# Performance work log

Measured on AMD Instinct MI355X. Metric: run time of the kernel, lower is better.

## Reference

```python
import jax, jax.numpy as jnp
import numpy as np

B, T, E, H, V, C, L = 32, 512, 512, 512, 50000, 32, 2


def _lstm_dir(x, Wih, Whh, bih, bhh, reverse):
    # x: (B,T,in). Precompute the big input GEMM once; scan only does h @ Whh^T.
    xw = jnp.einsum('bti,gi->btg', x, Wih) + bih + bhh  # (B,T,4H)
    Hd = Whh.shape[1]
    Bd = x.shape[0]

    def step(carry, xt):
        h, c = carry
        g = xt + h @ Whh.T
        i, f, gg, o = jnp.split(g, 4, axis=-1)  # torch gate order i,f,g,o
        c = jax.nn.sigmoid(f) * c + jax.nn.sigmoid(i) * jnp.tanh(gg)
        h = jax.nn.sigmoid(o) * jnp.tanh(c)
        return (h, c), h

    init = (jnp.zeros((Bd, Hd), x.dtype), jnp.zeros((Bd, Hd), x.dtype))
    _, hs = jax.lax.scan(step, init, jnp.swapaxes(xw, 0, 1), reverse=reverse)
    return jnp.swapaxes(hs, 0, 1)  # (B,T,H), time-aligned for both directions


def setup_inputs() -> dict:
    key = jax.random.key(0)
    keys = jax.random.split(key, 40)

    def u(k, shape, scale):
        return jax.random.uniform(k, shape, jnp.float32, -scale, scale)

    s = 1.0 / np.sqrt(H)
    inp = {
        'x': jax.random.randint(keys[0], (B, T), 0, V),
        'truth': jax.random.uniform(keys[1], (B, T, 1), jnp.float32),
        'teacher_forcing': 1,
        'emb': jax.random.normal(keys[2], (V, E), jnp.float32),
    }
    ki = 3
    for l in range(L):
        insz = E if l == 0 else 2 * H
        for d in ('f', 'b'):
            inp[f'Wih{l}{d}'] = u(keys[ki], (4 * H, insz), s); ki += 1
            inp[f'Whh{l}{d}'] = u(keys[ki], (4 * H, H), s); ki += 1
            inp[f'bih{l}{d}'] = u(keys[ki], (4 * H,), s); ki += 1
            inp[f'bhh{l}{d}'] = u(keys[ki], (4 * H,), s); ki += 1
    sc = 1.0 / np.sqrt(2 * H + 1)
    inp['Wc'] = u(keys[ki], (C, 2 * H + 1), sc); ki += 1
    inp['bc'] = u(keys[ki], (C,), sc)
    return inp


def reference(x, truth, teacher_forcing, emb,
              Wih0f, Whh0f, bih0f, bhh0f, Wih0b, Whh0b, bih0b, bhh0b,
              Wih1f, Whh1f, bih1f, bhh1f, Wih1b, Whh1b, bih1b, bhh1b,
              Wc, bc):
    h = emb[x]  # (B,T,E)
    layer_params = [
        ((Wih0f, Whh0f, bih0f, bhh0f), (Wih0b, Whh0b, bih0b, bhh0b)),
        ((Wih1f, Whh1f, bih1f, bhh1f), (Wih1b, Whh1b, bih1b, bhh1b)),
    ]
    for pf, pb in layer_params:
        out_f = _lstm_dir(h, *pf, reverse=False)
        out_b = _lstm_dir(h, *pb, reverse=True)
        h = jnp.concatenate([out_f, out_b], axis=-1)  # (B,T,2H)
    # past feature: zeros at t=0; truth[:, t-1] when teacher forcing, else zeros
    zero0 = jnp.zeros((h.shape[0], 1, 1), h.dtype)
    if teacher_forcing:
        past = jnp.concatenate([zero0, truth[:, :-1, :]], axis=1)  # (B,T,1)
    else:
        past = jnp.zeros((h.shape[0], h.shape[1], 1), h.dtype)
    feat = jnp.concatenate([past, h], axis=-1)  # (B,T,2H+1)
    logits = jnp.einsum('btf,cf->btc', feat, Wc) + bc
    y = jax.nn.log_softmax(logits, axis=-1)  # softmax over classes (intended math)
    return jnp.swapaxes(y, 1, 2)  # (B, classes, T)
```

## Files before the change

### kernel.cpp

```cpp
#include <hip/hip_runtime.h>


#define BB 32
#define TT 512
#define EE 512
#define HH 512
#define NG 2048
#define CC 32

typedef __attribute__((ext_vector_type(8))) short short8v;
typedef __attribute__((ext_vector_type(4))) float float4v;
typedef unsigned long long u64;

__device__ __forceinline__ float bf2f(unsigned short u) {
    return __uint_as_float(((unsigned)u) << 16);
}
__device__ __forceinline__ float bf_lo(unsigned u) { return __uint_as_float(u << 16); }
__device__ __forceinline__ float bf_hi(unsigned u) { return __uint_as_float(u & 0xffff0000u); }
__device__ __forceinline__ unsigned short f2bf(float f) {
    unsigned u = __float_as_uint(f);
    u += 0x7fffu + ((u >> 16) & 1u);
    return (unsigned short)(u >> 16);
}
__device__ __forceinline__ float fast_sigmoid(float x) {
    return 1.f / (1.f + __expf(-x));
}
__device__ __forceinline__ float fast_tanh(float x) {
    x = fminf(fmaxf(x, -15.f), 15.f);
    float e = __expf(2.f * x);
    return (e - 1.f) / (e + 1.f);
}

__global__ __launch_bounds__(256)
void embed_k(const int* __restrict__ x, const float* __restrict__ emb,
             unsigned short* __restrict__ h0) {
    int idx = blockIdx.x * 256 + threadIdx.x;
    int row = idx >> 7;
    int c4  = idx & 127;
    int tok = x[row];
    float4 v = *(const float4*)(emb + ((size_t)tok << 9) + (c4 << 2));
    ushort4 o;
    o.x = f2bf(v.x); o.y = f2bf(v.y); o.z = f2bf(v.z); o.w = f2bf(v.w);
    *(ushort4*)(h0 + ((size_t)row << 9) + (c4 << 2)) = o;
}

__global__ __launch_bounds__(256)
void gemm_xw(const unsigned short* __restrict__ A, const float* __restrict__ Bw,
             const float* __restrict__ bih, const float* __restrict__ bhh,
             unsigned short* __restrict__ Cp, int M, int K) {
    __shared__ unsigned short As[64][40];
    __shared__ unsigned short Bs[64][40];
    const int bn = blockIdx.x & 31, bm = blockIdx.x >> 5;
    const int tid = threadIdx.x;
    const int wv = tid >> 6, lane = tid & 63;
    const int wm = (wv >> 1) * 32, wn = (wv & 1) * 32;
    const int sr = tid >> 2, sk = (tid & 3) * 8;
    const int fr = lane & 15, fk = (lane >> 4) * 8;

    float4v acc[2][2];
#pragma unroll
    for (int i = 0; i < 2; ++i)
#pragma unroll
        for (int j = 0; j < 2; ++j) acc[i][j] = (float4v)(0.0f);

    for (int k0 = 0; k0 < K; k0 += 32) {
        *(uint4*)&As[sr][sk] = *(const uint4*)(A + (size_t)(bm * 64 + sr) * K + k0 + sk);
        const float* bp = Bw + (size_t)(bn * 64 + sr) * K + k0 + sk;
        const float4 b0 = *(const float4*)bp;
        const float4 b1 = *(const float4*)(bp + 4);
        ushort4 o0 = {f2bf(b0.x), f2bf(b0.y), f2bf(b0.z), f2bf(b0.w)};
        ushort4 o1 = {f2bf(b1.x), f2bf(b1.y), f2bf(b1.z), f2bf(b1.w)};
        *(ushort4*)&Bs[sr][sk] = o0;
        *(ushort4*)&Bs[sr][sk + 4] = o1;
        __syncthreads();

        short8v a0 = *(const short8v*)&As[wm + fr][fk];
        short8v a1 = *(const short8v*)&As[wm + 16 + fr][fk];
        short8v bb0 = *(const short8v*)&Bs[wn + fr][fk];
        short8v bb1 = *(const short8v*)&Bs[wn + 16 + fr][fk];
        acc[0][0] = __builtin_amdgcn_mfma_f32_16x16x32_bf16(a0, bb0, acc[0][0], 0, 0, 0);
        acc[0][1] = __builtin_amdgcn_mfma_f32_16x16x32_bf16(a0, bb1, acc[0][1], 0, 0, 0);
        acc[1][0] = __builtin_amdgcn_mfma_f32_16x16x32_bf16(a1, bb0, acc[1][0], 0, 0, 0);
        acc[1][1] = __builtin_amdgcn_mfma_f32_16x16x32_bf16(a1, bb1, acc[1][1], 0, 0, 0);
        __syncthreads();
    }

    const int r4 = (lane >> 4) * 4;
#pragma unroll
    for (int nt = 0; nt < 2; ++nt) {
        const int nglob = bn * 64 + wn + nt * 16 + fr;
        const float bias = bih[nglob] + bhh[nglob];
        const int gate = nglob >> 9;
        const int jbv = (nglob & 511) >> 4;
        const int loc = gate * 16 + (nglob & 15);
#pragma unroll
        for (int mt = 0; mt < 2; ++mt) {
#pragma unroll
            for (int i = 0; i < 4; ++i) {
                const int mglob = bm * 64 + wm + mt * 16 + r4 + i;
                const int b = mglob >> 9, t = mglob & 511;
                Cp[(((size_t)jbv * 512 + t) * 32 + b) * 64 + loc] =
                    f2bf(acc[mt][nt][i] + bias);
            }
        }
    }
}

__global__ __launch_bounds__(256, 1)
void lstm_scan(const float* __restrict__ WhhF, const float* __restrict__ WhhB,
               const unsigned short* __restrict__ xwF, const unsigned short* __restrict__ xwB,
               unsigned short* __restrict__ outcat,
               u64* __restrict__ h_pp) {
    __shared__ __align__(16) unsigned char hs[16384];
    __shared__ float gsh[4][8][16];
    __shared__ unsigned xsh[2][256];

    const int blk = blockIdx.x;
    const int grp = blk & 7, jb = blk >> 3;
    const int bg = grp & 3, dir = grp >> 2;
    const int tid = threadIdx.x;
    const int wv = tid >> 6, lane = tid & 63;
    const float* Whh = dir ? WhhB : WhhF;
    const unsigned short* xw = dir ? xwB : xwF;
    const int js = jb << 4;

    short8v bw[16];
    {
        const float* wrow = Whh + (size_t)(wv * 512 + js + (lane & 15)) * HH
                            + (lane >> 4) * 8;
#pragma unroll
        for (int kk = 0; kk < 16; ++kk) {
            const float4 f0 = *(const float4*)(wrow + kk * 32);
            const float4 f1 = *(const float4*)(wrow + kk * 32 + 4);
            short8v b;
            b[0] = (short)f2bf(f0.x); b[1] = (short)f2bf(f0.y);
            b[2] = (short)f2bf(f0.z); b[3] = (short)f2bf(f0.w);
            b[4] = (short)f2bf(f1.x); b[5] = (short)f2bf(f1.y);
            b[6] = (short)f2bf(f1.z); b[7] = (short)f2bf(f1.w);
            bw[kk] = b;
        }
    }

    for (int i = tid; i < 8 * 64; i += 256) {
        int r = 8 + (i >> 6), c = i & 63;
        *(uint4*)(hs + r * 1024 + ((c * 16) ^ ((r & 7) << 4))) = make_uint4(0, 0, 0, 0);
    }

    float c_st = 0.f;
    const int srow = tid >> 5, kcol = tid & 31;
    const unsigned swz_w = (srow & 7) << 4;
    const int arow = lane & 15, ag16 = (lane >> 4) * 16;
    const unsigned swz_r = (arow & 7) << 4;
    __syncthreads();

    for (int t = 0; t < TT; ++t) {
        const int tt = dir ? (TT - 1 - t) : t;

        const unsigned xv = *(const unsigned*)(
            xw + (((size_t)jb * 512 + tt) * 32 + bg * 8) * 64 + 2 * tid);

        {
            const u64* hsrc =
                h_pp + ((size_t)((t & 3) * 2 + dir) * BB + bg * 8 + srow) * 256;
            const unsigned sq = (unsigned)t;
            u64 v0, v1, v2, v3, v4, v5, v6, v7;
            for (;;) {
                v0 = __hip_atomic_load(hsrc + kcol,       __ATOMIC_RELAXED, __HIP_MEMORY_SCOPE_AGENT);
                v1 = __hip_atomic_load(hsrc + kcol + 32,  __ATOMIC_RELAXED, __HIP_MEMORY_SCOPE_AGENT);
                v2 = __hip_atomic_load(hsrc + kcol + 64,  __ATOMIC_RELAXED, __HIP_MEMORY_SCOPE_AGENT);
                v3 = __hip_atomic_load(hsrc + kcol + 96,  __ATOMIC_RELAXED, __HIP_MEMORY_SCOPE_AGENT);
                v4 = __hip_atomic_load(hsrc + kcol + 128, __ATOMIC_RELAXED, __HIP_MEMORY_SCOPE_AGENT);
                v5 = __hip_atomic_load(hsrc + kcol + 160, __ATOMIC_RELAXED, __HIP_MEMORY_SCOPE_AGENT);
                v6 = __hip_atomic_load(hsrc + kcol + 192, __ATOMIC_RELAXED, __HIP_MEMORY_SCOPE_AGENT);
                v7 = __hip_atomic_load(hsrc + kcol + 224, __ATOMIC_RELAXED, __HIP_MEMORY_SCOPE_AGENT);
                unsigned ok = ((unsigned)(v0 >> 32) == sq) & ((unsigned)(v1 >> 32) == sq)
                            & ((unsigned)(v2 >> 32) == sq) & ((unsigned)(v3 >> 32) == sq)
                            & ((unsigned)(v4 >> 32) == sq) & ((unsigned)(v5 >> 32) == sq)
                            & ((unsigned)(v6 >> 32) == sq) & ((unsigned)(v7 >> 32) == sq);
                if (ok) break;
                __builtin_amdgcn_s_sleep(1);
            }
            xsh[t & 1][tid] = xv;
            unsigned char* hrow = hs + srow * 1024;
            *(unsigned*)(hrow + ((4 * kcol +   0) ^ swz_w)) = (unsigned)v0;
            *(unsigned*)(hrow + ((4 * kcol + 128) ^ swz_w)) = (unsigned)v1;
            *(unsigned*)(hrow + ((4 * kcol + 256) ^ swz_w)) = (unsigned)v2;
            *(unsigned*)(hrow + ((4 * kcol + 384) ^ swz_w)) = (unsigned)v3;
            *(unsigned*)(hrow + ((4 * kcol + 512) ^ swz_w)) = (unsigned)v4;
            *(unsigned*)(hrow + ((4 * kcol + 640) ^ swz_w)) = (unsigned)v5;
            *(unsigned*)(hrow + ((4 * kcol + 768) ^ swz_w)) = (unsigned)v6;
            *(unsigned*)(hrow + ((4 * kcol + 896) ^ swz_w)) = (unsigned)v7;
        }
        __syncthreads();

        {
            float4v a0 = (float4v)(0.0f), a1 = (float4v)(0.0f);
#pragma unroll
            for (int kk = 0; kk < 16; kk += 2) {
                short8v af0 = *(const short8v*)(hs + arow * 1024 +
                                  (((kk * 64) + ag16) ^ swz_r));
                short8v af1 = *(const short8v*)(hs + arow * 1024 +
                                  ((((kk + 1) * 64) + ag16) ^ swz_r));
                a0 = __builtin_amdgcn_mfma_f32_16x16x32_bf16(af0, bw[kk], a0, 0, 0, 0);
                a1 = __builtin_amdgcn_mfma_f32_16x16x32_bf16(af1, bw[kk + 1], a1, 0, 0, 0);
            }
            if (lane < 32) {
#pragma unroll
                for (int reg = 0; reg < 4; ++reg) {
                    gsh[wv][(lane >> 4) * 4 + reg][lane & 15] = a0[reg] + a1[reg];
                }
            }
        }
        __syncthreads();

        if (tid < 128) {
            const int bl = tid >> 4, jj = tid & 15;
            const unsigned short* xp = (const unsigned short*)xsh[t & 1];
            const int vb = bl * 64 + jj;
            float gi = gsh[0][bl][jj] + bf2f(xp[vb]);
            float gf = gsh[1][bl][jj] + bf2f(xp[vb + 16]);
            float gg = gsh[2][bl][jj] + bf2f(xp[vb + 32]);
            float go = gsh[3][bl][jj] + bf2f(xp[vb + 48]);
            float si = fast_sigmoid(gi);
            float sf = fast_sigmoid(gf);
            float so = fast_sigmoid(go);
            c_st = sf * c_st + si * fast_tanh(gg);
            float hv = so * fast_tanh(c_st);
            const unsigned short hb16 = f2bf(hv);
            const int b_glob = bg * 8 + bl;
            unsigned hv32 = hb16;
            unsigned other = (unsigned)__shfl_xor((int)hv32, 1);
            if (!(tid & 1)) {
                u64 pkt = ((u64)(unsigned)(t + 1) << 32) | (u64)(hv32 | (other << 16));
                __hip_atomic_store(
                    &h_pp[((size_t)(((t + 1) & 3) * 2 + dir) * BB + b_glob) * 256
                          + jb * 8 + (jj >> 1)],
                    pkt, __ATOMIC_RELAXED, __HIP_MEMORY_SCOPE_AGENT);
            }
            outcat[((size_t)b_glob * TT + tt) * 1024 + dir * HH + js + jj] = hb16;
        }
    }
}

__global__ __launch_bounds__(256)
void classifier_k(const unsigned short* __restrict__ hcat, const float* __restrict__ truth,
                  const int* __restrict__ tf, const float* __restrict__ Wc,
                  const float* __restrict__ bc, float* __restrict__ out) {
    __shared__ float feat[8][1024];
    __shared__ float featp[8];
    const int tid = threadIdx.x;
    const int bt0 = blockIdx.x * 8;
    for (int i = tid; i < 8 * 128; i += 256) {
        int bl = i >> 7, ch = i & 127;
        uint4 u = *(const uint4*)(hcat + (size_t)(bt0 + bl) * 1024 + ch * 8);
        *(float4*)&feat[bl][ch * 8] = make_float4(bf_lo(u.x), bf_hi(u.x), bf_lo(u.y), bf_hi(u.y));
        *(float4*)&feat[bl][ch * 8 + 4] = make_float4(bf_lo(u.z), bf_hi(u.z), bf_lo(u.w), bf_hi(u.w));
    }
    if (tid < 8) {
        int bt = bt0 + tid;
        int t = bt & 511;
        featp[tid] = (t > 0 && tf[0] != 0) ? truth[bt - 1] : 0.f;
    }
    __syncthreads();
    const int bl = tid >> 5, c = tid & 31;
    const int bt = bt0 + bl;
    float acc = featp[bl] * Wc[c * 1025] + bc[c];
    const float* w = Wc + c * 1025 + 1;
    for (int f4 = 0; f4 < 256; ++f4) {
        const float4 fv = *(const float4*)&feat[bl][f4 * 4];
        acc = fmaf(fv.x, w[f4 * 4 + 0],
              fmaf(fv.y, w[f4 * 4 + 1],
              fmaf(fv.z, w[f4 * 4 + 2],
              fmaf(fv.w, w[f4 * 4 + 3], acc))));
    }
    float m = acc;
#pragma unroll
    for (int mk = 16; mk; mk >>= 1) m = fmaxf(m, __shfl_xor(m, mk));
    float e = expf(acc - m);
    float s = e;
#pragma unroll
    for (int mk = 16; mk; mk >>= 1) s += __shfl_xor(s, mk);
    float lse = m + logf(s);
    int b = bt >> 9, t = bt & 511;
    out[((size_t)b * CC + c) * TT + t] = acc - lse;
}

extern "C" void kernel_launch(void* const* d_in, const int* in_sizes, int n_in,
                              void* d_out, int out_size, void* d_ws, size_t ws_size,
                              hipStream_t stream) {
    const int* x = (const int*)d_in[0];
    const float* truth = (const float*)d_in[1];
    const int* tf = (const int*)d_in[2];
    const float* emb = (const float*)d_in[3];
    const float* Wih0f = (const float*)d_in[4];
    const float* Whh0f = (const float*)d_in[5];
    const float* bih0f = (const float*)d_in[6];
    const float* bhh0f = (const float*)d_in[7];
    const float* Wih0b = (const float*)d_in[8];
    const float* Whh0b = (const float*)d_in[9];
    const float* bih0b = (const float*)d_in[10];
    const float* bhh0b = (const float*)d_in[11];
    const float* Wih1f = (const float*)d_in[12];
    const float* Whh1f = (const float*)d_in[13];
    const float* bih1f = (const float*)d_in[14];
    const float* bhh1f = (const float*)d_in[15];
    const float* Wih1b = (const float*)d_in[16];
    const float* Whh1b = (const float*)d_in[17];
    const float* bih1b = (const float*)d_in[18];
    const float* bhh1b = (const float*)d_in[19];
    const float* Wc = (const float*)d_in[20];
    const float* bc = (const float*)d_in[21];
    float* out = (float*)d_out;

    const size_t off_h0  = 0;
    const size_t off_xwf = 16777216;
    const size_t off_xwb = off_xwf + 67108864;
    const size_t off_hc1 = off_xwb + 67108864;
    const size_t off_hc2 = off_hc1 + 33554432;
    const size_t off_hpp = off_hc2 + 33554432;
    const size_t need = off_hpp + 524288;
    if (ws_size < need) return;

    char* ws = (char*)d_ws;
    unsigned short* h0  = (unsigned short*)(ws + off_h0);
    unsigned short* xwf = (unsigned short*)(ws + off_xwf);
    unsigned short* xwb = (unsigned short*)(ws + off_xwb);
    unsigned short* hc1 = (unsigned short*)(ws + off_hc1);
    unsigned short* hc2 = (unsigned short*)(ws + off_hc2);
    u64*            hpp = (u64*)(ws + off_hpp);

    embed_k<<<8192, 256, 0, stream>>>(x, emb, h0);

    gemm_xw<<<8192, 256, 0, stream>>>(h0, Wih0f, bih0f, bhh0f, xwf, BB * TT, EE);
    gemm_xw<<<8192, 256, 0, stream>>>(h0, Wih0b, bih0b, bhh0b, xwb, BB * TT, EE);
    (void)hipMemsetAsync(ws + off_hpp, 0, 524288, stream);
    lstm_scan<<<256, 256, 0, stream>>>(Whh0f, Whh0b, xwf, xwb, hc1, hpp);

    gemm_xw<<<8192, 256, 0, stream>>>(hc1, Wih1f, bih1f, bhh1f, xwf, BB * TT, 1024);
    gemm_xw<<<8192, 256, 0, stream>>>(hc1, Wih1b, bih1b, bhh1b, xwb, BB * TT, 1024);
    (void)hipMemsetAsync(ws + off_hpp, 0, 524288, stream);
    lstm_scan<<<256, 256, 0, stream>>>(Whh1f, Whh1b, xwf, xwb, hc2, hpp);

    classifier_k<<<2048, 256, 0, stream>>>(hc2, truth, tf, Wc, bc, out);
}
```

Baseline: 3.177 ms.

## Enlarge GEMM tiles with swizzled LDS and prefetch xw in LSTM scan

The input-projection GEMM moves from 64x64 tiles with K=32 to 128x128 tiles with K=64, using 512 threads and XOR-swizzled shared memory, which gives more MFMA work per barrier and more reuse of each loaded tile. The LSTM scan now prefetches the next timestep's xw value during the current step's compute instead of loading it inside the loop, and skips the sleep on the first failed poll of the h exchange. Several stores and loads become nontemporal. The larger GEMM tile raises register and LDS pressure, and the 2048-block grid is still large enough to fill the device.

```diff
diff --git a/kernel.cpp b/kernel.cpp
--- a/kernel.cpp
+++ b/kernel.cpp
@@ -21,6 +21,9 @@
     unsigned u = __float_as_uint(f);
     u += 0x7fffu + ((u >> 16) & 1u);
     return (unsigned short)(u >> 16);
+}
+__device__ __forceinline__ unsigned pk2(float a, float b) {
+    return (unsigned)f2bf(a) | ((unsigned)f2bf(b) << 16);
 }
 __device__ __forceinline__ float fast_sigmoid(float x) {
     return 1.f / (1.f + __expf(-x));
@@ -44,63 +47,85 @@
     *(ushort4*)(h0 + ((size_t)row << 9) + (c4 << 2)) = o;
 }
 
-__global__ __launch_bounds__(256)
+__global__ __launch_bounds__(512)
 void gemm_xw(const unsigned short* __restrict__ A, const float* __restrict__ Bw,
              const float* __restrict__ bih, const float* __restrict__ bhh,
              unsigned short* __restrict__ Cp, int M, int K) {
-    __shared__ unsigned short As[64][40];
-    __shared__ unsigned short Bs[64][40];
-    const int bn = blockIdx.x & 31, bm = blockIdx.x >> 5;
+    __shared__ __align__(16) unsigned char As[128 * 128];
+    __shared__ __align__(16) unsigned char Bs[128 * 128];
+    const int bn = blockIdx.x & 15, bm = blockIdx.x >> 4;
     const int tid = threadIdx.x;
     const int wv = tid >> 6, lane = tid & 63;
-    const int wm = (wv >> 1) * 32, wn = (wv & 1) * 32;
-    const int sr = tid >> 2, sk = (tid & 3) * 8;
-    const int fr = lane & 15, fk = (lane >> 4) * 8;
-
-    float4v acc[2][2];
-#pragma unroll
-    for (int i = 0; i < 2; ++i)
-#pragma unroll
-        for (int j = 0; j < 2; ++j) acc[i][j] = (float4v)(0.0f);
-
-    for (int k0 = 0; k0 < K; k0 += 32) {
-        *(uint4*)&As[sr][sk] = *(const uint4*)(A + (size_t)(bm * 64 + sr) * K + k0 + sk);
-        const float* bp = Bw + (size_t)(bn * 64 + sr) * K + k0 + sk;
-        const float4 b0 = *(const float4*)bp;
-        const float4 b1 = *(const float4*)(bp + 4);
-        ushort4 o0 = {f2bf(b0.x), f2bf(b0.y), f2bf(b0.z), f2bf(b0.w)};
-        ushort4 o1 = {f2bf(b1.x), f2bf(b1.y), f2bf(b1.z), f2bf(b1.w)};
-        *(ushort4*)&Bs[sr][sk] = o0;
-        *(ushort4*)&Bs[sr][sk + 4] = o1;
+    const int wr = wv >> 2, wc = wv & 3;
+    const int srow = tid >> 2, skc = (tid & 3) * 16;
+    const unsigned sswz = (srow & 7) << 4;
+    const int fr = lane & 15, fkb = (lane >> 4) * 16;
+
+    float4v acc[4][2];
+#pragma unroll
+    for (int i = 0; i < 4; ++i) { acc[i][0] = (float4v)(0.f); acc[i][1] = (float4v)(0.f); }
+
+    const unsigned short* arow_p = A + (size_t)(bm * 128 + srow) * K + skc;
+    const float* brow_p = Bw + (size_t)(bn * 128 + srow) * K + skc;
+    unsigned char* const as_row = As + srow * 128;
+    unsigned char* const bs_row = Bs + srow * 128;
+    const int sb0 = skc * 2;
+
+    for (int k0 = 0; k0 < K; k0 += 64) {
+        uint4 a0 = *(const uint4*)(arow_p + k0);
+        uint4 a1 = *(const uint4*)(arow_p + k0 + 8);
+        float4 b0 = *(const float4*)(brow_p + k0);
+        float4 b1 = *(const float4*)(brow_p + k0 + 4);
+        float4 b2 = *(const float4*)(brow_p + k0 + 8);
+        float4 b3 = *(const float4*)(brow_p + k0 + 12);
+        *(uint4*)(as_row + ((sb0     ) ^ sswz)) = a0;
+        *(uint4*)(as_row + ((sb0 + 16) ^ sswz)) = a1;
+        uint4 bp0 = make_uint4(pk2(b0.x, b0.y), pk2(b0.z, b0.w), pk2(b1.x, b1.y), pk2(b1.z, b1.w));
+        uint4 bp1 = make_uint4(pk2(b2.x, b2.y), pk2(b2.z, b2.w), pk2(b3.x, b3.y), pk2(b3.z, b3.w));
+        *(uint4*)(bs_row + ((sb0     ) ^ sswz)) = bp0;
+        *(uint4*)(bs_row + ((sb0 + 16) ^ sswz)) = bp1;
         __syncthreads();
 
-        short8v a0 = *(const short8v*)&As[wm + fr][fk];
-        short8v a1 = *(const short8v*)&As[wm + 16 + fr][fk];
-        short8v bb0 = *(const short8v*)&Bs[wn + fr][fk];
-        short8v bb1 = *(const short8v*)&Bs[wn + 16 + fr][fk];
-        acc[0][0] = __builtin_amdgcn_mfma_f32_16x16x32_bf16(a0, bb0, acc[0][0], 0, 0, 0);
-        acc[0][1] = __builtin_amdgcn_mfma_f32_16x16x32_bf16(a0, bb1, acc[0][1], 0, 0, 0);
-        acc[1][0] = __builtin_amdgcn_mfma_f32_16x16x32_bf16(a1, bb0, acc[1][0], 0, 0, 0);
-        acc[1][1] = __builtin_amdgcn_mfma_f32_16x16x32_bf16(a1, bb1, acc[1][1], 0, 0, 0);
+#pragma unroll
+        for (int kt = 0; kt < 2; ++kt) {
+            const int cb = kt * 64 + fkb;
+            short8v af[4], bf[2];
+#pragma unroll
+            for (int mt = 0; mt < 4; ++mt) {
+                const int r = wr * 64 + mt * 16 + fr;
+                af[mt] = *(const short8v*)(As + r * 128 + (cb ^ ((r & 7) << 4)));
+            }
+#pragma unroll
+            for (int nt = 0; nt < 2; ++nt) {
+                const int r = wc * 32 + nt * 16 + fr;
+                bf[nt] = *(const short8v*)(Bs + r * 128 + (cb ^ ((r & 7) << 4)));
+            }
+#pragma unroll
+            for (int mt = 0; mt < 4; ++mt) {
+                acc[mt][0] = __builtin_amdgcn_mfma_f32_16x16x32_bf16(af[mt], bf[0], acc[mt][0], 0, 0, 0);
+                acc[mt][1] = __builtin_amdgcn_mfma_f32_16x16x32_bf16(af[mt], bf[1], acc[mt][1], 0, 0, 0);
+            }
+        }
         __syncthreads();
     }
 
     const int r4 = (lane >> 4) * 4;
 #pragma unroll
     for (int nt = 0; nt < 2; ++nt) {
-        const int nglob = bn * 64 + wn + nt * 16 + fr;
+        const int nglob = bn * 128 + wc * 32 + nt * 16 + fr;
         const float bias = bih[nglob] + bhh[nglob];
         const int gate = nglob >> 9;
         const int jbv = (nglob & 511) >> 4;
         const int loc = gate * 16 + (nglob & 15);
 #pragma unroll
-        for (int mt = 0; mt < 2; ++mt) {
+        for (int mt = 0; mt < 4; ++mt) {
 #pragma unroll
             for (int i = 0; i < 4; ++i) {
-                const int mglob = bm * 64 + wm + mt * 16 + r4 + i;
+                const int mglob = bm * 128 + wr * 64 + mt * 16 + r4 + i;
                 const int b = mglob >> 9, t = mglob & 511;
-                Cp[(((size_t)jbv * 512 + t) * 32 + b) * 64 + loc] =
-                    f2bf(acc[mt][nt][i] + bias);
+                __builtin_nontemporal_store(
+                    f2bf(acc[mt][nt][i] + bias),
+                    &Cp[(((size_t)jbv * 512 + t) * 32 + b) * 64 + loc]);
             }
         }
     }
@@ -113,7 +138,7 @@
                u64* __restrict__ h_pp) {
     __shared__ __align__(16) unsigned char hs[16384];
     __shared__ float gsh[4][8][16];
-    __shared__ unsigned xsh[2][256];
+    __shared__ unsigned xsh[256];
 
     const int blk = blockIdx.x;
     const int grp = blk & 7, jb = blk >> 3;
@@ -153,17 +178,19 @@
     const unsigned swz_r = (arow & 7) << 4;
     __syncthreads();
 
+    unsigned xv_cur = __builtin_nontemporal_load((const unsigned*)(
+        xw + (((size_t)jb * 512 + (dir ? TT - 1 : 0)) * 32 + bg * 8) * 64 + 2 * tid));
+    unsigned xv_next = 0;
+
     for (int t = 0; t < TT; ++t) {
         const int tt = dir ? (TT - 1 - t) : t;
-
-        const unsigned xv = *(const unsigned*)(
-            xw + (((size_t)jb * 512 + tt) * 32 + bg * 8) * 64 + 2 * tid);
 
         {
             const u64* hsrc =
                 h_pp + ((size_t)((t & 3) * 2 + dir) * BB + bg * 8 + srow) * 256;
             const unsigned sq = (unsigned)t;
             u64 v0, v1, v2, v3, v4, v5, v6, v7;
+            int tries = 0;
             for (;;) {
                 v0 = __hip_atomic_load(hsrc + kcol,       __ATOMIC_RELAXED, __HIP_MEMORY_SCOPE_AGENT);
                 v1 = __hip_atomic_load(hsrc + kcol + 32,  __ATOMIC_RELAXED, __HIP_MEMORY_SCOPE_AGENT);
@@ -178,9 +205,8 @@
                             & ((unsigned)(v4 >> 32) == sq) & ((unsigned)(v5 >> 32) == sq)
                             & ((unsigned)(v6 >> 32) == sq) & ((unsigned)(v7 >> 32) == sq);
                 if (ok) break;
-                __builtin_amdgcn_s_sleep(1);
-            }
-            xsh[t & 1][tid] = xv;
+                if (tries++) __builtin_amdgcn_s_sleep(1);
+            }
             unsigned char* hrow = hs + srow * 1024;
             *(unsigned*)(hrow + ((4 * kcol +   0) ^ swz_w)) = (unsigned)v0;
             *(unsigned*)(hrow + ((4 * kcol + 128) ^ swz_w)) = (unsigned)v1;
@@ -193,6 +219,13 @@
         }
         __syncthreads();
 
+        xsh[tid] = xv_cur;
+        if (t + 1 < TT) {
+            const int ttn = dir ? (TT - 2 - t) : (t + 1);
+            xv_next = __builtin_nontemporal_load((const unsigned*)(
+                xw + (((size_t)jb * 512 + ttn) * 32 + bg * 8) * 64 + 2 * tid));
+        }
+
         {
             float4v a0 = (float4v)(0.0f), a1 = (float4v)(0.0f);
 #pragma unroll
@@ -215,7 +248,7 @@
 
         if (tid < 128) {
             const int bl = tid >> 4, jj = tid & 15;
-            const unsigned short* xp = (const unsigned short*)xsh[t & 1];
+            const unsigned short* xp = (const unsigned short*)xsh;
             const int vb = bl * 64 + jj;
             float gi = gsh[0][bl][jj] + bf2f(xp[vb]);
             float gf = gsh[1][bl][jj] + bf2f(xp[vb + 16]);
@@ -237,8 +270,10 @@
                           + jb * 8 + (jj >> 1)],
                     pkt, __ATOMIC_RELAXED, __HIP_MEMORY_SCOPE_AGENT);
             }
-            outcat[((size_t)b_glob * TT + tt) * 1024 + dir * HH + js + jj] = hb16;
-        }
+            __builtin_nontemporal_store(
+                hb16, &outcat[((size_t)b_glob * TT + tt) * 1024 + dir * HH + js + jj]);
+        }
+        xv_cur = xv_next;
     }
 }
 
@@ -331,13 +366,13 @@
 
     embed_k<<<8192, 256, 0, stream>>>(x, emb, h0);
 
-    gemm_xw<<<8192, 256, 0, stream>>>(h0, Wih0f, bih0f, bhh0f, xwf, BB * TT, EE);
-    gemm_xw<<<8192, 256, 0, stream>>>(h0, Wih0b, bih0b, bhh0b, xwb, BB * TT, EE);
+    gemm_xw<<<2048, 512, 0, stream>>>(h0, Wih0f, bih0f, bhh0f, xwf, BB * TT, EE);
+    gemm_xw<<<2048, 512, 0, stream>>>(h0, Wih0b, bih0b, bhh0b, xwb, BB * TT, EE);
     (void)hipMemsetAsync(ws + off_hpp, 0, 524288, stream);
     lstm_scan<<<256, 256, 0, stream>>>(Whh0f, Whh0b, xwf, xwb, hc1, hpp);
 
-    gemm_xw<<<8192, 256, 0, stream>>>(hc1, Wih1f, bih1f, bhh1f, xwf, BB * TT, 1024);
-    gemm_xw<<<8192, 256, 0, stream>>>(hc1, Wih1b, bih1b, bhh1b, xwb, BB * TT, 1024);
+    gemm_xw<<<2048, 512, 0, stream>>>(hc1, Wih1f, bih1f, bhh1f, xwf, BB * TT, 1024);
+    gemm_xw<<<2048, 512, 0, stream>>>(hc1, Wih1b, bih1b, bhh1b, xwb, BB * TT, 1024);
     (void)hipMemsetAsync(ws + off_hpp, 0, 524288, stream);
     lstm_scan<<<256, 256, 0, stream>>>(Whh1f, Whh1b, xwf, xwb, hc2, hpp);
 
```

Result: slower. 3.712 ms (+16.9%).
